# Performance work log

Measured on AMD Instinct MI355X. Metric: run time of the kernel, lower is better.

Reference implementation:

```python
import jax, jax.numpy as jnp
import numpy as np
from math import isqrt

NUM_HEADS = 8
EPS = 1e-12  # torch F.normalize default eps


def _l2_normalize_seq(t):
    # normalize over the sequence axis (dim=-2), matching F.normalize(t, dim=-2)
    n = jnp.sqrt(jnp.sum(t * t, axis=-2, keepdims=True))
    return t / jnp.maximum(n, EPS)


def setup_inputs() -> dict:
    key = jax.random.key(0)
    ks = jax.random.split(key, 7)
    B, L, C = 8, 4096, 384
    s = 0.02
    return {
        "x": jax.random.normal(ks[0], (B, L, C), jnp.float32),
        "qkv_w": jax.random.normal(ks[1], (3 * C, C), jnp.float32) * s,
        "qkv_b": jax.random.normal(ks[2], (3 * C,), jnp.float32) * s,
        "proj_w": jax.random.normal(ks[3], (C, C), jnp.float32) * s,
        "proj_b": jax.random.normal(ks[4], (C,), jnp.float32) * s,
        "temperature": jnp.ones((NUM_HEADS, 1, 1), jnp.float32),
        "conv_w": jax.random.normal(ks[5], (C, 1, 3, 3), jnp.float32) * s,
        "conv_b": jax.random.normal(ks[6], (C,), jnp.float32) * s,
    }


def reference(x, qkv_w, qkv_b, proj_w, proj_b, temperature, conv_w, conv_b):
    B, L, C = x.shape
    h = NUM_HEADS
    d = C // h
    H = W = isqrt(L)

    # qkv projection -> (3, B, h, L, d)
    qkv = (x @ qkv_w.T + qkv_b).reshape(B, L, 3, h, d).transpose(2, 0, 3, 1, 4)
    q, k, v = qkv[0], qkv[1], qkv[2]

    # L2 normalize q, k over sequence axis
    q = _l2_normalize_seq(q)
    k = _l2_normalize_seq(k)

    # LePE: depthwise 3x3 conv on v in image layout (B, C, H, W)
    v_img = v.transpose(0, 1, 3, 2).reshape(B, C, H, W)
    lepe = jax.lax.conv_general_dilated(
        v_img, conv_w, window_strides=(1, 1), padding=((1, 1), (1, 1)),
        feature_group_count=C,
        dimension_numbers=("NCHW", "OIHW", "NCHW"),
    ) + conv_b[None, :, None, None]
    lepe = lepe.reshape(B, h, d, L).transpose(0, 1, 3, 2)  # (B, h, L, d)

    # linear attention: attn = (k^T v) * temperature, shape (B, h, d, d)
    attn = jnp.einsum("bhld,bhle->bhde", k, v) * temperature
    out = jnp.einsum("bhld,bhde->bhle", q, attn) + lepe  # (B, h, L, d)

    out = out.transpose(0, 2, 1, 3).reshape(B, L, C)
    out = out @ proj_w.T + proj_b
    return (out, attn)
```

## Files before the change

### kernel.cpp

```cpp
#include <hip/hip_runtime.h>
#include <hip/hip_bf16.h>


typedef __bf16 bf16x8 __attribute__((ext_vector_type(8)));
typedef float f32x4 __attribute__((ext_vector_type(4)));

__device__ inline __bf16 f2b(float f) {
    __hip_bfloat16 h = __float2bfloat16(f);
    __bf16 r; __builtin_memcpy(&r, &h, 2); return r;
}
__device__ inline float b2f(__hip_bfloat16 h) { return __bfloat162float(h); }
__device__ inline float b2f(__bf16 v) {
    __hip_bfloat16 h; __builtin_memcpy(&h, &v, 2); return __bfloat162float(h);
}

__device__ inline bf16x8 load8(const __hip_bfloat16* p) {
    uint4 v = *(const uint4*)p;
    bf16x8 r; __builtin_memcpy(&r, &v, 16); return r;
}
__device__ inline bf16x8 load8(const float* p) {
    float4 a = *(const float4*)p;
    float4 b = *(const float4*)(p + 4);
    bf16x8 r;
    r[0] = f2b(a.x); r[1] = f2b(a.y); r[2] = f2b(a.z); r[3] = f2b(a.w);
    r[4] = f2b(b.x); r[5] = f2b(b.y); r[6] = f2b(b.z); r[7] = f2b(b.w);
    return r;
}

__device__ inline void storef(float* p, float v) { *p = v; }
__device__ inline void storef(__hip_bfloat16* p, float v) { *p = __float2bfloat16(v); }

__device__ inline void gl_lds16(const __hip_bfloat16* g, __hip_bfloat16* l) {
    __builtin_amdgcn_global_load_lds(
        (const __attribute__((address_space(1))) void*)g,
        (__attribute__((address_space(3))) void*)l,
        16, 0, 0);
}

__global__ __launch_bounds__(256) void cvt_kernel(
    const float* __restrict__ x,  __hip_bfloat16* __restrict__ xb,
    const float* __restrict__ qw, __hip_bfloat16* __restrict__ qwb,
    const float* __restrict__ pw, __hip_bfloat16* __restrict__ pwb)
{
    int blk = blockIdx.x;
    const float* src; __hip_bfloat16* dst; int base;
    if (blk < 6144)      { src = x;  dst = xb;  base = blk; }
    else if (blk < 6360) { src = qw; dst = qwb; base = blk - 6144; }
    else                 { src = pw; dst = pwb; base = blk - 6360; }
    int i = base * 256 + threadIdx.x;
    bf16x8 v = load8(src + (size_t)i * 8);
    *(bf16x8*)(dst + (size_t)i * 8) = v;
}

template <typename TO>
__global__ __launch_bounds__(256) void gemm_bf16_nt(
    const __hip_bfloat16* __restrict__ A,
    const __hip_bfloat16* __restrict__ Bw,
    const float* __restrict__ bias,
    TO* __restrict__ C,
    int M, int N, int K)
{
    __shared__ __hip_bfloat16 As[128 * 32];
    __shared__ __hip_bfloat16 Bs[128 * 32];
    const int t = threadIdx.x;
    const int w = t >> 6, lane = t & 63;
    const int r16 = lane & 15, quad = lane >> 4;
    const int m0 = blockIdx.y * 128, n0 = blockIdx.x * 128;
    const int wm = w >> 1, wn = w & 1;
    const int srow = lane >> 2;
    const int scol = (lane & 3) * 8;

    f32x4 acc[4][4];
    #pragma unroll
    for (int mi = 0; mi < 4; ++mi)
        #pragma unroll
        for (int ni = 0; ni < 4; ++ni)
            acc[mi][ni] = (f32x4){0.f, 0.f, 0.f, 0.f};

    for (int k0 = 0; k0 < K; k0 += 32) {
        #pragma unroll
        for (int p = 0; p < 2; ++p) {
            int row = w * 32 + p * 16 + srow;
            gl_lds16(A  + (size_t)(m0 + row) * K + k0 + scol, &As[row * 32 + scol]);
            gl_lds16(Bw + (size_t)(n0 + row) * K + k0 + scol, &Bs[row * 32 + scol]);
        }
        __syncthreads();
        bf16x8 af[4], bfr[4];
        #pragma unroll
        for (int mi = 0; mi < 4; ++mi)
            af[mi] = *(const bf16x8*)&As[(wm * 64 + mi * 16 + r16) * 32 + quad * 8];
        #pragma unroll
        for (int ni = 0; ni < 4; ++ni)
            bfr[ni] = *(const bf16x8*)&Bs[(wn * 64 + ni * 16 + r16) * 32 + quad * 8];
        #pragma unroll
        for (int mi = 0; mi < 4; ++mi)
            #pragma unroll
            for (int ni = 0; ni < 4; ++ni)
                acc[mi][ni] = __builtin_amdgcn_mfma_f32_16x16x32_bf16(af[mi], bfr[ni], acc[mi][ni], 0, 0, 0);
        __syncthreads();
    }

    #pragma unroll
    for (int ni = 0; ni < 4; ++ni) {
        int col = n0 + wn * 64 + ni * 16 + r16;
        float bv = bias[col];
        #pragma unroll
        for (int mi = 0; mi < 4; ++mi) {
            #pragma unroll
            for (int reg = 0; reg < 4; ++reg) {
                int row = m0 + wm * 64 + mi * 16 + quad * 4 + reg;
                storef(&C[(size_t)row * N + col], acc[mi][ni][reg] + bv);
            }
        }
    }
}

__global__ __launch_bounds__(256) void colsumsq_kernel(
    const __hip_bfloat16* __restrict__ qkv, float* __restrict__ sumsq)
{
    int b  = blockIdx.y;
    int l0 = blockIdx.x * 64;
    int t  = threadIdx.x;
    const __hip_bfloat16* base = qkv + (size_t)(b * 4096 + l0) * 1152;
    #pragma unroll
    for (int p = 0; p < 3; ++p) {
        int c = p * 256 + t;
        float acc = 0.f;
        for (int r = 0; r < 64; ++r) {
            float v = b2f(base[(size_t)r * 1152 + c]);
            acc += v * v;
        }
        atomicAdd(&sumsq[b * 768 + c], acc);
    }
}

__global__ void invnorm_kernel(const float* __restrict__ sumsq, float* __restrict__ invn)
{
    int i = blockIdx.x * 256 + threadIdx.x;
    if (i < 6144) invn[i] = 1.f / fmaxf(sqrtf(sumsq[i]), 1e-12f);
}

__global__ __launch_bounds__(256) void ktv_mfma_kernel(
    const __hip_bfloat16* __restrict__ qkv, float* __restrict__ G)
{
    __shared__ __hip_bfloat16 kT[4][48][40];
    __shared__ __hip_bfloat16 vT[4][48][40];
    __shared__ float red[4][48][49];

    const int bh = blockIdx.y; const int b = bh >> 3; const int h = bh & 7;
    const int lbase = blockIdx.x * 1024;
    const int t = threadIdx.x;
    const int w = t >> 6, lane = t & 63;
    const int r16 = lane & 15, quad = lane >> 4;

    f32x4 acc[3][3];
    #pragma unroll
    for (int mi = 0; mi < 3; ++mi)
        #pragma unroll
        for (int ni = 0; ni < 3; ++ni)
            acc[mi][ni] = (f32x4){0.f, 0.f, 0.f, 0.f};

    const int mat  = t & 1;
    const int lrow = t >> 1;
    const int tile = lrow >> 5, l_in = lrow & 31;
    const __hip_bfloat16* src = qkv + 384 + mat * 384 + h * 48;
    __hip_bfloat16* dstT = (mat ? &vT[0][0][0] : &kT[0][0][0]) + ((size_t)tile * 48 * 40 + l_in);

    for (int it = 0; it < 8; ++it) {
        const int l0 = lbase + it * 128;
        const __hip_bfloat16* p = src + (size_t)(b * 4096 + l0 + lrow) * 1152;
        __hip_bfloat16 row[48];
        #pragma unroll
        for (int j = 0; j < 6; ++j) {
            uint4 v = *(const uint4*)(p + j * 8);
            __builtin_memcpy(&row[j * 8], &v, 16);
        }
        #pragma unroll
        for (int d = 0; d < 48; ++d)
            dstT[d * 40] = row[d];
        __syncthreads();

        bf16x8 af[3], bfr[3];
        #pragma unroll
        for (int mi = 0; mi < 3; ++mi)
            af[mi] = *(const bf16x8*)&kT[w][mi * 16 + r16][quad * 8];
        #pragma unroll
        for (int ni = 0; ni < 3; ++ni)
            bfr[ni] = *(const bf16x8*)&vT[w][ni * 16 + r16][quad * 8];
        #pragma unroll
        for (int mi = 0; mi < 3; ++mi)
            #pragma unroll
            for (int ni = 0; ni < 3; ++ni)
                acc[mi][ni] = __builtin_amdgcn_mfma_f32_16x16x32_bf16(af[mi], bfr[ni], acc[mi][ni], 0, 0, 0);
        __syncthreads();
    }

    #pragma unroll
    for (int mi = 0; mi < 3; ++mi)
        #pragma unroll
        for (int ni = 0; ni < 3; ++ni)
            #pragma unroll
            for (int reg = 0; reg < 4; ++reg)
                red[w][mi * 16 + quad * 4 + reg][ni * 16 + r16] = acc[mi][ni][reg];
    __syncthreads();

    float* Gb = G + (size_t)bh * 2304;
    for (int cell = t; cell < 2304; cell += 256) {
        int row = cell / 48, col = cell % 48;
        float s = red[0][row][col] + red[1][row][col] + red[2][row][col] + red[3][row][col];
        atomicAdd(&Gb[cell], s);
    }
}

__global__ void scale_attn_kernel(
    const float* __restrict__ G, const float* __restrict__ invn,
    const float* __restrict__ temp,
    float* __restrict__ attn_out, float* __restrict__ attn2)
{
    int bh = blockIdx.x; int b = bh >> 3; int h = bh & 7;
    float tf = temp[h];
    int t = threadIdx.x;
    for (int e = t; e < 2304; e += 256) {
        int dk = e / 48;
        float ink = invn[b * 768 + 384 + h * 48 + dk];
        float inq = invn[b * 768 + h * 48 + dk];
        float av  = G[(size_t)bh * 2304 + e] * ink * tf;
        attn_out[(size_t)bh * 2304 + e] = av;
        attn2[(size_t)bh * 2304 + e]    = av * inq;
    }
}

__global__ __launch_bounds__(256) void qattn_lepe_mfma(
    const __hip_bfloat16* __restrict__ qkv, const float* __restrict__ attn2,
    const float* __restrict__ conv_w, const float* __restrict__ conv_b,
    __hip_bfloat16* __restrict__ y)
{
    __shared__ __attribute__((aligned(16))) char smem[26624];
    __hip_bfloat16 (*qs)[72]  = (__hip_bfloat16 (*)[72])smem;
    __hip_bfloat16 (*a2s)[72] = (__hip_bfloat16 (*)[72])(smem + 18432);
    float (*ys)[52]           = (float (*)[52])smem;
    __shared__ __hip_bfloat16 vs[4][64][48];
    __shared__ float cwT[9][48];
    __shared__ float cb[48];

    const int bh = blockIdx.y; const int b = bh >> 3; const int h = bh & 7;
    const int yi0 = blockIdx.x * 2;
    const int l0  = yi0 * 64;
    const int t = threadIdx.x;
    const int w = t >> 6, lane = t & 63;
    const int r16 = lane & 15, quad = lane >> 4;

    const __hip_bfloat16* qbase = qkv + (size_t)(b * 4096 + l0) * 1152 + h * 48;
    #pragma unroll
    for (int i = 0; i < 3; ++i) {
        int chunk = t + i * 256;
        int row = chunk / 6, cg = chunk % 6;
        *(bf16x8*)&qs[row][cg * 8] = load8(qbase + (size_t)row * 1152 + cg * 8);
    }
    *(bf16x8*)&qs[t >> 1][48 + (t & 1) * 8] = (bf16x8)0;

    const float* a2g = attn2 + (size_t)bh * 2304;
    for (int i = t; i < 3072; i += 256) {
        int e = i >> 6, dd = i & 63;
        float val = (dd < 48) ? a2g[dd * 48 + e] : 0.f;
        a2s[e][dd] = __float2bfloat16(val);
    }

    const __hip_bfloat16* vbase = qkv + (size_t)b * 4096 * 1152 + 768 + h * 48;
    #pragma unroll
    for (int i = 0; i < 6; ++i) {
        int chunk = t + i * 256;
        int r = chunk / 384, rem = chunk % 384;
        int xx = rem / 6, cg = rem % 6;
        int yy = yi0 - 1 + r;
        bf16x8 v = (yy >= 0 && yy < 64)
            ? load8(vbase + (size_t)(yy * 64 + xx) * 1152 + cg * 8)
            : (bf16x8)0;
        *(bf16x8*)&vs[r][xx][cg * 8] = v;
    }

    for (int i = t; i < 432; i += 256)
        cwT[i / 48][i % 48] = conv_w[(h * 48 + (i % 48)) * 9 + (i / 48)];
    if (t < 48) cb[t] = conv_b[h * 48 + t];
    __syncthreads();

    f32x4 acc[2][3];
    #pragma unroll
    for (int mi = 0; mi < 2; ++mi)
        #pragma unroll
        for (int ni = 0; ni < 3; ++ni)
            acc[mi][ni] = (f32x4){0.f, 0.f, 0.f, 0.f};
    #pragma unroll
    for (int ks = 0; ks < 2; ++ks) {
        int kb = ks * 32 + quad * 8;
        bf16x8 af[2], bfr[3];
        #pragma unroll
        for (int mi = 0; mi < 2; ++mi)
            af[mi] = *(const bf16x8*)&qs[w * 32 + mi * 16 + r16][kb];
        #pragma unroll
        for (int ni = 0; ni < 3; ++ni)
            bfr[ni] = *(const bf16x8*)&a2s[ni * 16 + r16][kb];
        #pragma unroll
        for (int mi = 0; mi < 2; ++mi)
            #pragma unroll
            for (int ni = 0; ni < 3; ++ni)
                acc[mi][ni] = __builtin_amdgcn_mfma_f32_16x16x32_bf16(af[mi], bfr[ni], acc[mi][ni], 0, 0, 0);
    }
    __syncthreads();

    #pragma unroll
    for (int mi = 0; mi < 2; ++mi)
        #pragma unroll
        for (int ni = 0; ni < 3; ++ni)
            #pragma unroll
            for (int reg = 0; reg < 4; ++reg)
                ys[w * 32 + mi * 16 + quad * 4 + reg][ni * 16 + r16] = acc[mi][ni][reg];
    __syncthreads();

    __hip_bfloat16* ybase = y + (size_t)(b * 4096 + l0) * 384 + h * 48;
    #pragma unroll
    for (int i = 0; i < 3; ++i) {
        int g = t + i * 256;
        int l_in = g / 6, cg = g % 6, e0 = cg * 8;
        int xi = l_in & 63, vr0 = l_in >> 6;
        float o[8];
        #pragma unroll
        for (int j = 0; j < 8; ++j) o[j] = ys[l_in][e0 + j] + cb[e0 + j];
        #pragma unroll
        for (int dy = 0; dy < 3; ++dy) {
            #pragma unroll
            for (int dx = 0; dx < 3; ++dx) {
                int xx = xi + dx - 1;
                if (xx < 0 || xx > 63) continue;
                bf16x8 vv = *(const bf16x8*)&vs[vr0 + dy][xx][e0];
                const float* cwp = &cwT[dy * 3 + dx][e0];
                #pragma unroll
                for (int j = 0; j < 8; ++j) o[j] += b2f(vv[j]) * cwp[j];
            }
        }
        __hip_bfloat16 ob[8];
        #pragma unroll
        for (int j = 0; j < 8; ++j) ob[j] = __float2bfloat16(o[j]);
        uint4 pk; __builtin_memcpy(&pk, ob, 16);
        *(uint4*)(ybase + (size_t)l_in * 384 + e0) = pk;
    }
}

extern "C" void kernel_launch(void* const* d_in, const int* in_sizes, int n_in,
                              void* d_out, int out_size, void* d_ws, size_t ws_size,
                              hipStream_t stream)
{
    const float* x      = (const float*)d_in[0];
    const float* qkv_w  = (const float*)d_in[1];
    const float* qkv_b  = (const float*)d_in[2];
    const float* proj_w = (const float*)d_in[3];
    const float* proj_b = (const float*)d_in[4];
    const float* temp   = (const float*)d_in[5];
    const float* conv_w = (const float*)d_in[6];
    const float* conv_b = (const float*)d_in[7];

    char* ws = (char*)d_ws;
    __hip_bfloat16* qkv = (__hip_bfloat16*)(ws);
    __hip_bfloat16* yb  = (__hip_bfloat16*)(ws + 75497472);
    float* sumsq = (float*)(ws + 100663296);
    float* G     = (float*)(ws + 100687872);
    float* invn  = (float*)(ws + 101277696);
    float* attn2 = (float*)(ws + 101302272);
    __hip_bfloat16* x_bf16  = yb;
    __hip_bfloat16* qkv_wb  = (__hip_bfloat16*)(ws + 101892096);
    __hip_bfloat16* proj_wb = (__hip_bfloat16*)(ws + 102776832);

    float* out      = (float*)d_out;
    float* attn_out = out + 12582912;

    (void)hipMemsetAsync(ws + 100663296, 0, 614400, stream);

    cvt_kernel<<<6432, 256, 0, stream>>>(x, x_bf16, qkv_w, qkv_wb, proj_w, proj_wb);
    gemm_bf16_nt<__hip_bfloat16><<<dim3(9, 256), 256, 0, stream>>>(
        x_bf16, qkv_wb, qkv_b, qkv, 32768, 1152, 384);
    colsumsq_kernel<<<dim3(64, 8), 256, 0, stream>>>(qkv, sumsq);
    invnorm_kernel<<<24, 256, 0, stream>>>(sumsq, invn);
    ktv_mfma_kernel<<<dim3(4, 64), 256, 0, stream>>>(qkv, G);
    scale_attn_kernel<<<64, 256, 0, stream>>>(G, invn, temp, attn_out, attn2);
    qattn_lepe_mfma<<<dim3(32, 64), 256, 0, stream>>>(qkv, attn2, conv_w, conv_b, yb);
    gemm_bf16_nt<float><<<dim3(3, 256), 256, 0, stream>>>(
        yb, proj_wb, proj_b, out, 32768, 384, 384);
}
```

Before: 265.1 us.

## Fuse q/k column sum-of-squares into QKV GEMM epilogue and remap blocks per XCD

Removes the separate colsumsq kernel by computing squared column sums in the QKV GEMM epilogue, reduced with wave shuffles and an atomicAdd per column per tile. The grid becomes 1D, with block indices remapped so consecutive blocks on each XCD share M tiles, which is meant to improve cache locality. This saves one full read of the q/k part of the QKV buffer and one kernel launch. In exchange it adds more atomics and sums the fp32 values before bf16 rounding, a slight numerical difference from the old path.

After: 256.8 us. -3.1%, faster.

```diff
diff --git a/kernel.cpp b/kernel.cpp
--- a/kernel.cpp
+++ b/kernel.cpp
@@ -58,14 +58,19 @@
     const __hip_bfloat16* __restrict__ Bw,
     const float* __restrict__ bias,
     TO* __restrict__ C,
-    int M, int N, int K)
+    int N, int K, int NXT,
+    float* __restrict__ sq)
 {
     __shared__ __hip_bfloat16 As[128 * 32];
     __shared__ __hip_bfloat16 Bs[128 * 32];
     const int t = threadIdx.x;
     const int w = t >> 6, lane = t & 63;
     const int r16 = lane & 15, quad = lane >> 4;
-    const int m0 = blockIdx.y * 128, n0 = blockIdx.x * 128;
+    const int bx  = blockIdx.x;
+    const int xcd = bx & 7, seq = bx >> 3;
+    const int n_t = seq % NXT, m_t = seq / NXT;
+    const int m0 = (xcd + 8 * m_t) * 128;
+    const int n0 = n_t * 128;
     const int wm = w >> 1, wn = w & 1;
     const int srow = lane >> 2;
     const int scol = (lane & 3) * 8;
@@ -104,33 +109,25 @@
     for (int ni = 0; ni < 4; ++ni) {
         int col = n0 + wn * 64 + ni * 16 + r16;
         float bv = bias[col];
+        float s = 0.f;
         #pragma unroll
         for (int mi = 0; mi < 4; ++mi) {
             #pragma unroll
             for (int reg = 0; reg < 4; ++reg) {
                 int row = m0 + wm * 64 + mi * 16 + quad * 4 + reg;
-                storef(&C[(size_t)row * N + col], acc[mi][ni][reg] + bv);
+                float o = acc[mi][ni][reg] + bv;
+                storef(&C[(size_t)row * N + col], o);
+                s += o * o;
             }
         }
-    }
-}
-
-__global__ __launch_bounds__(256) void colsumsq_kernel(
-    const __hip_bfloat16* __restrict__ qkv, float* __restrict__ sumsq)
-{
-    int b  = blockIdx.y;
-    int l0 = blockIdx.x * 64;
-    int t  = threadIdx.x;
-    const __hip_bfloat16* base = qkv + (size_t)(b * 4096 + l0) * 1152;
-    #pragma unroll
-    for (int p = 0; p < 3; ++p) {
-        int c = p * 256 + t;
-        float acc = 0.f;
-        for (int r = 0; r < 64; ++r) {
-            float v = b2f(base[(size_t)r * 1152 + c]);
-            acc += v * v;
-        }
-        atomicAdd(&sumsq[b * 768 + c], acc);
+        if (sq != nullptr && col < 768) {
+            s += __shfl_xor(s, 16);
+            s += __shfl_xor(s, 32);
+            if (quad == 0) {
+                int b = m0 >> 12;
+                atomicAdd(&sq[b * 768 + col], s);
+            }
+        }
     }
 }
 
@@ -376,13 +373,12 @@
     (void)hipMemsetAsync(ws + 100663296, 0, 614400, stream);
 
     cvt_kernel<<<6432, 256, 0, stream>>>(x, x_bf16, qkv_w, qkv_wb, proj_w, proj_wb);
-    gemm_bf16_nt<__hip_bfloat16><<<dim3(9, 256), 256, 0, stream>>>(
-        x_bf16, qkv_wb, qkv_b, qkv, 32768, 1152, 384);
-    colsumsq_kernel<<<dim3(64, 8), 256, 0, stream>>>(qkv, sumsq);
+    gemm_bf16_nt<__hip_bfloat16><<<2304, 256, 0, stream>>>(
+        x_bf16, qkv_wb, qkv_b, qkv, 1152, 384, 9, sumsq);
     invnorm_kernel<<<24, 256, 0, stream>>>(sumsq, invn);
     ktv_mfma_kernel<<<dim3(4, 64), 256, 0, stream>>>(qkv, G);
     scale_attn_kernel<<<64, 256, 0, stream>>>(G, invn, temp, attn_out, attn2);
     qattn_lepe_mfma<<<dim3(32, 64), 256, 0, stream>>>(qkv, attn2, conv_w, conv_b, yb);
-    gemm_bf16_nt<float><<<dim3(3, 256), 256, 0, stream>>>(
-        yb, proj_wb, proj_b, out, 32768, 384, 384);
-}
+    gemm_bf16_nt<float><<<768, 256, 0, stream>>>(
+        yb, proj_wb, proj_b, out, 384, 384, 3, nullptr);
+}
```
